# Performance work log

Hardware: AMD Instinct MI355X
Metric: run time of the kernel (lower is better)

Reference implementation:

```python
import jax, jax.numpy as jnp
import numpy as np

B, T, D_MODEL = 2, 1024, 1024
H, DEPTH = 8, 5
DH = D_MODEL // H


def setup_inputs() -> dict:
    key = jax.random.key(0)
    k_x, k_wp, k_bp, k_wv, k_wo = jax.random.split(key, 5)
    x = jax.random.normal(k_x, (B, T, D_MODEL), dtype=jnp.float32)
    # Parameters stored as [in, out] (y = x @ W + b), equivalent math to nn.Linear.
    Wp = jax.random.normal(k_wp, (D_MODEL, H * DEPTH), dtype=jnp.float32) * 0.02
    bp = jnp.zeros((H * DEPTH,), dtype=jnp.float32)
    Wv = jax.random.normal(k_wv, (D_MODEL, D_MODEL), dtype=jnp.float32) * 0.02
    Wo = jax.random.normal(k_wo, (D_MODEL, D_MODEL), dtype=jnp.float32) * 0.02
    return {"x": x, "Wp": Wp, "bp": bp, "Wv": Wv, "Wo": Wo}


def reference(x, Wp, bp, Wv, Wo):
    Bx, Tx, d = x.shape
    # soft binary path decisions: B,H,T,DEPTH
    paths = jax.nn.sigmoid(x @ Wp + bp)              # B,T,H*DEPTH
    paths = paths.reshape(Bx, Tx, H, DEPTH).transpose(0, 2, 1, 3)  # B,H,T,DEPTH
    # pairwise per-level agreement: B,H,Tq,Tk,DEPTH
    pq = paths[:, :, :, None, :]
    pk = paths[:, :, None, :, :]
    agree = pq * pk + (1.0 - pq) * (1.0 - pk)
    # shared-prefix length via cumprod over depth, summed
    sim = jnp.cumprod(agree, axis=-1).sum(axis=-1) / DEPTH  # B,H,Tq,Tk
    # causal mask
    mask = jnp.triu(jnp.ones((Tx, Tx), dtype=bool), k=1)
    sim = jnp.where(mask[None, None], -jnp.inf, sim)
    attn = jax.nn.softmax(sim, axis=-1)              # B,H,T,T
    V = (x @ Wv).reshape(Bx, Tx, H, DH).transpose(0, 2, 1, 3)  # B,H,T,dh
    ctx = jnp.einsum('bhqk,bhkd->bhqd', attn, V)
    ctx = ctx.transpose(0, 2, 1, 3).reshape(Bx, Tx, d)
    return ctx @ Wo
```

## Files before the change

kernel.cpp:

```cpp
#include <hip/hip_runtime.h>
#include <hip/hip_bf16.h>

#define B_ 2
#define T_ 1024
#define D_ 1024
#define H_ 8
#define DEPTH_ 5
#define DH_ 128

typedef short s16x8 __attribute__((ext_vector_type(8)));
typedef short s16x4 __attribute__((ext_vector_type(4)));
typedef float f32x4 __attribute__((ext_vector_type(4)));

__device__ inline short f2bf(float f) {
  __hip_bfloat16 h = __float2bfloat16(f);
  return *reinterpret_cast<short*>(&h);
}

typedef __attribute__((address_space(3))) unsigned int lds_u32_t;
typedef __attribute__((address_space(1))) unsigned int glb_u32_t;
__device__ __forceinline__ void glds16(const void* g, void* l) {
  __builtin_amdgcn_global_load_lds((const glb_u32_t*)g, (lds_u32_t*)l, 16, 0,
                                   0);
}

__global__ __launch_bounds__(256) void prep_kernel(
    const float* __restrict__ Wv, const float* __restrict__ Wo,
    const float* __restrict__ Wp, const float* __restrict__ x,
    short* __restrict__ WBt, short* __restrict__ Wot,
    short* __restrict__ xb) {
  int tid = threadIdx.x;
  if (blockIdx.z < 2) {
    const float* W = blockIdx.z ? Wo : Wv;
    short* Wt = blockIdx.z ? Wot : WBt;
    __shared__ float tile[64][65];
    int k0 = blockIdx.y * 64, n0 = blockIdx.x * 64;
#pragma unroll
    for (int i = 0; i < 4; ++i) {
      int idx = tid + i * 256;
      int r = idx >> 4, c4 = (idx & 15) * 4;
      float4 v = *(const float4*)&W[(size_t)(k0 + r) * D_ + n0 + c4];
      tile[r][c4 + 0] = v.x;
      tile[r][c4 + 1] = v.y;
      tile[r][c4 + 2] = v.z;
      tile[r][c4 + 3] = v.w;
    }
    __syncthreads();
#pragma unroll
    for (int j = 0; j < 2; ++j) {
      int idx = tid + j * 256;
      int n = idx >> 3, k8 = (idx & 7) * 8;
      s16x8 outv;
#pragma unroll
      for (int jj = 0; jj < 8; ++jj) outv[jj] = f2bf(tile[k8 + jj][n]);
      *(s16x8*)&Wt[(size_t)(n0 + n) * D_ + k0 + k8] = outv;
    }
  } else {
    int bid = blockIdx.y * 16 + blockIdx.x;
#pragma unroll
    for (int c = 0; c < 4; ++c) {
      size_t idx = (size_t)bid * 8192 + c * 2048 + tid * 8;
      float4 f0 = *(const float4*)&x[idx];
      float4 f1 = *(const float4*)&x[idx + 4];
      s16x8 v;
      v[0] = f2bf(f0.x); v[1] = f2bf(f0.y);
      v[2] = f2bf(f0.z); v[3] = f2bf(f0.w);
      v[4] = f2bf(f1.x); v[5] = f2bf(f1.y);
      v[6] = f2bf(f1.z); v[7] = f2bf(f1.w);
      *(s16x8*)&xb[idx] = v;
    }
    if (bid < 4) {
#pragma unroll
      for (int it = 0; it < 8; ++it) {
        int item = bid * 2048 + it * 256 + tid;
        int row = item >> 7, k8 = (item & 127) * 8;
        s16x8 v;
        if (row < H_ * DEPTH_) {
#pragma unroll
          for (int j = 0; j < 8; ++j)
            v[j] = f2bf(Wp[(size_t)(k8 + j) * (H_ * DEPTH_) + row]);
        } else {
#pragma unroll
          for (int j = 0; j < 8; ++j) v[j] = 0;
        }
        *(s16x8*)&WBt[(size_t)(1024 + row) * D_ + k8] = v;
      }
    }
  }
}

template <int MODE>
__global__ __launch_bounds__(256) void gemm128(
    const short* __restrict__ A, const short* __restrict__ Bt,
    float* __restrict__ Cf, const float* __restrict__ bp,
    short* __restrict__ Vt, float* __restrict__ paths_t) {
  __shared__ short As[64 * 128];
  __shared__ short Bs[64 * 128];
  const int K = D_;
  int tid = threadIdx.x;
  int bm = blockIdx.y << 6, bn = blockIdx.x << 6;
  int w = tid >> 6, lane = tid & 63;
  int wm = (w >> 1) * 32, wn = (w & 1) * 32;
  int g = lane >> 4, fr = lane & 15;
  f32x4 acc[2][2] = {{{0.f, 0.f, 0.f, 0.f}, {0.f, 0.f, 0.f, 0.f}},
                     {{0.f, 0.f, 0.f, 0.f}, {0.f, 0.f, 0.f, 0.f}}};

  int r4 = lane >> 4;
  int cg = lane & 15;
  const short* Asrc[4];
  const short* Bsrc[4];
  short* Adst[4];
  short* Bdst[4];
#pragma unroll
  for (int i = 0; i < 4; ++i) {
    int row = w * 16 + i * 4 + r4;
    int scol = (cg ^ (row & 15)) * 8;
    Asrc[i] = A + (size_t)(bm + row) * K + scol;
    Bsrc[i] = Bt + (size_t)(bn + row) * K + scol;
    Adst[i] = &As[(w * 16 + i * 4) * 128];
    Bdst[i] = &Bs[(w * 16 + i * 4) * 128];
  }

  for (int k0 = 0; k0 < K; k0 += 128) {
    __syncthreads();
#pragma unroll
    for (int i = 0; i < 4; ++i) {
      glds16(Asrc[i] + k0, Adst[i]);
      glds16(Bsrc[i] + k0, Bdst[i]);
    }
    __syncthreads();
#pragma unroll
    for (int ks = 0; ks < 4; ++ks) {
      int p = (((ks * 4 + g) ^ fr)) * 8;
      s16x8 a0 = *(const s16x8*)&As[(wm + fr) * 128 + p];
      s16x8 a1 = *(const s16x8*)&As[(wm + 16 + fr) * 128 + p];
      s16x8 b0 = *(const s16x8*)&Bs[(wn + fr) * 128 + p];
      s16x8 b1 = *(const s16x8*)&Bs[(wn + 16 + fr) * 128 + p];
      acc[0][0] = __builtin_amdgcn_mfma_f32_16x16x32_bf16(a0, b0, acc[0][0], 0, 0, 0);
      acc[0][1] = __builtin_amdgcn_mfma_f32_16x16x32_bf16(a0, b1, acc[0][1], 0, 0, 0);
      acc[1][0] = __builtin_amdgcn_mfma_f32_16x16x32_bf16(a1, b0, acc[1][0], 0, 0, 0);
      acc[1][1] = __builtin_amdgcn_mfma_f32_16x16x32_bf16(a1, b1, acc[1][1], 0, 0, 0);
    }
  }
  int col = lane & 15, rbase = (lane >> 4) * 4;
  if (MODE == 0) {
#pragma unroll
    for (int mi = 0; mi < 2; ++mi)
#pragma unroll
      for (int ni = 0; ni < 2; ++ni)
#pragma unroll
        for (int r = 0; r < 4; ++r)
          Cf[(size_t)(bm + wm + mi * 16 + rbase + r) * D_ + bn + wn +
             ni * 16 + col] = acc[mi][ni][r];
  } else if (bn < 1024) {
#pragma unroll
    for (int mi = 0; mi < 2; ++mi)
#pragma unroll
      for (int ni = 0; ni < 2; ++ni) {
        int m = bm + wm + mi * 16 + rbase;
        int n = bn + wn + ni * 16 + col;
        int b = m >> 10, t = m & (T_ - 1);
        int h = n >> 7, dh = n & (DH_ - 1);
        s16x4 v4;
#pragma unroll
        for (int r = 0; r < 4; ++r) v4[r] = f2bf(acc[mi][ni][r]);
        *(s16x4*)&Vt[((size_t)((b * H_ + h) * DH_ + dh)) * T_ + t] = v4;
      }
  } else {
#pragma unroll
    for (int ni = 0; ni < 2; ++ni) {
      int pn = wn + ni * 16 + col;
      if (pn < H_ * DEPTH_) {
        float bias = bp[pn];
        int h = pn / DEPTH_, d = pn % DEPTH_;
#pragma unroll
        for (int mi = 0; mi < 2; ++mi)
#pragma unroll
          for (int r = 0; r < 4; ++r) {
            int m = bm + wm + mi * 16 + rbase + r;
            int b = m >> 10, t = m & (T_ - 1);
            float p = 1.f / (1.f + __expf(-(acc[mi][ni][r] + bias)));
            paths_t[(((size_t)(b * H_ + h) * T_ + t) * DEPTH_) + d] = p;
          }
      }
    }
  }
}

#define LS2 136

__global__ __launch_bounds__(512) void attn_kernel(
    const float* __restrict__ paths_t, const short* __restrict__ Vt,
    short* __restrict__ ctxb) {
  int bh = blockIdx.y;
  int b = bh >> 3, h = bh & 7;
  int bx = blockIdx.x;
  int w = threadIdx.x >> 6, lane = threadIdx.x & 63;
  int g = lane >> 4, fr = lane & 15;

  __shared__ short Vs[DH_ * LS2];
  __shared__ short Ss[32 * LS2];
  __shared__ float lsum_s[32];

  const float* pb = paths_t + (size_t)bh * T_ * DEPTH_;
  const short* vb = Vt + (size_t)bh * DH_ * T_;

  for (int half = 0; half < 2; ++half) {
    int qt = half ? (31 - bx) : bx;
    int q0 = qt * 32;
    int nkt = (qt >> 2) + 1;

    float pq[4][DEPTH_], mq[4][DEPTH_];
#pragma unroll
    for (int j = 0; j < 4; ++j) {
      const float* qr = pb + (size_t)(q0 + w * 4 + j) * DEPTH_;
#pragma unroll
      for (int d = 0; d < DEPTH_; ++d) {
        pq[j][d] = qr[d];
        mq[j][d] = 1.f - pq[j][d];
      }
    }
    f32x4 acc[2] = {{0.f, 0.f, 0.f, 0.f}, {0.f, 0.f, 0.f, 0.f}};
    float part[4] = {};

    for (int kt = 0; kt < nkt; ++kt) {
      int k0 = kt * 128;
      __syncthreads();
#pragma unroll
      for (int i = 0; i < 4; ++i) {
        int c = threadIdx.x + i * 512;
        int dh = c >> 4, ko = (c & 15) * 8;
        *(s16x8*)&Vs[dh * LS2 + ko] =
            *(const s16x8*)&vb[(size_t)dh * T_ + k0 + ko];
      }
      int kA = k0 + lane, kB = k0 + 64 + lane;
      const float* krA = pb + (size_t)kA * DEPTH_;
      const float* krB = pb + (size_t)kB * DEPTH_;
      float pkA[DEPTH_], mkA[DEPTH_], pkB[DEPTH_], mkB[DEPTH_];
#pragma unroll
      for (int d = 0; d < DEPTH_; ++d) {
        pkA[d] = krA[d]; mkA[d] = 1.f - pkA[d];
        pkB[d] = krB[d]; mkB[d] = 1.f - pkB[d];
      }
#pragma unroll
      for (int j = 0; j < 4; ++j) {
        int qg = q0 + w * 4 + j;
        {
          float a0 = fmaf(pq[j][0], pkA[0], mq[j][0] * mkA[0]);
          float a1 = fmaf(pq[j][1], pkA[1], mq[j][1] * mkA[1]);
          float a2 = fmaf(pq[j][2], pkA[2], mq[j][2] * mkA[2]);
          float a3 = fmaf(pq[j][3], pkA[3], mq[j][3] * mkA[3]);
          float a4 = fmaf(pq[j][4], pkA[4], mq[j][4] * mkA[4]);
          float t4 = 1.f + a4;
          float t3 = fmaf(a3, t4, 1.f);
          float t2 = fmaf(a2, t3, 1.f);
          float t1 = fmaf(a1, t2, 1.f);
          float s = a0 * t1;
          float wv = (kA <= qg) ? __expf(s * 0.2f) : 0.f;
          part[j] += wv;
          Ss[(w * 4 + j) * LS2 + lane] = f2bf(wv);
        }
        {
          float a0 = fmaf(pq[j][0], pkB[0], mq[j][0] * mkB[0]);
          float a1 = fmaf(pq[j][1], pkB[1], mq[j][1] * mkB[1]);
          float a2 = fmaf(pq[j][2], pkB[2], mq[j][2] * mkB[2]);
          float a3 = fmaf(pq[j][3], pkB[3], mq[j][3] * mkB[3]);
          float a4 = fmaf(pq[j][4], pkB[4], mq[j][4] * mkB[4]);
          float t4 = 1.f + a4;
          float t3 = fmaf(a3, t4, 1.f);
          float t2 = fmaf(a2, t3, 1.f);
          float t1 = fmaf(a1, t2, 1.f);
          float s = a0 * t1;
          float wv = (kB <= qg) ? __expf(s * 0.2f) : 0.f;
          part[j] += wv;
          Ss[(w * 4 + j) * LS2 + 64 + lane] = f2bf(wv);
        }
      }
      __syncthreads();
#pragma unroll
      for (int ks = 0; ks < 4; ++ks) {
        int ko = ks * 32 + g * 8;
        s16x8 sa0 = *(const s16x8*)&Ss[fr * LS2 + ko];
        s16x8 sa1 = *(const s16x8*)&Ss[(16 + fr) * LS2 + ko];
        s16x8 vv = *(const s16x8*)&Vs[(w * 16 + fr) * LS2 + ko];
        acc[0] = __builtin_amdgcn_mfma_f32_16x16x32_bf16(sa0, vv, acc[0], 0, 0, 0);
        acc[1] = __builtin_amdgcn_mfma_f32_16x16x32_bf16(sa1, vv, acc[1], 0, 0, 0);
      }
    }
#pragma unroll
    for (int j = 0; j < 4; ++j) {
      float s = part[j];
#pragma unroll
      for (int off = 32; off >= 1; off >>= 1) s += __shfl_xor(s, off, 64);
      if (lane == j) lsum_s[w * 4 + j] = s;
    }
    __syncthreads();
    int col = lane & 15, rbase = g * 4;
#pragma unroll
    for (int qt2 = 0; qt2 < 2; ++qt2)
#pragma unroll
      for (int r = 0; r < 4; ++r) {
        int ql = qt2 * 16 + rbase + r;
        int dh = w * 16 + col;
        float val = acc[qt2][r] / lsum_s[ql];
        ctxb[(size_t)(b * T_ + q0 + ql) * D_ + h * DH_ + dh] = f2bf(val);
      }
  }
}

extern "C" void kernel_launch(void* const* d_in, const int* in_sizes, int n_in,
                              void* d_out, int out_size, void* d_ws,
                              size_t ws_size, hipStream_t stream) {
  const float* x = (const float*)d_in[0];
  const float* Wp = (const float*)d_in[1];
  const float* bp = (const float*)d_in[2];
  const float* Wv = (const float*)d_in[3];
  const float* Wo = (const float*)d_in[4];
  float* out = (float*)d_out;

  char* ws = (char*)d_ws;
  float* paths_t = (float*)ws;
  short* Vt = (short*)(ws + 327680);
  short* WBt = (short*)(ws + 4521984);
  short* Wot = (short*)(ws + 6750208);
  short* ctxb = (short*)(ws + 8847360);
  short* xb = (short*)(ws + 13041664);

  prep_kernel<<<dim3(16, 16, 3), 256, 0, stream>>>(Wv, Wo, Wp, x, WBt, Wot,
                                                   xb);
  gemm128<1><<<dim3(17, 32), 256, 0, stream>>>(xb, WBt, nullptr, bp, Vt,
                                               paths_t);
  attn_kernel<<<dim3(16, B_ * H_), 512, 0, stream>>>(paths_t, Vt, ctxb);
  gemm128<0><<<dim3(16, 32), 256, 0, stream>>>(ctxb, Wot, out, nullptr,
                                               nullptr, nullptr);
}
```

Before: 128.0 us.

## Fuse V-projection, attention and output GEMM into one cooperative persistent kernel

Replaces the three kernels that ran after prep (V/paths GEMM, attention, output GEMM) with a single cooperative kernel of 256 blocks that uses grid.sync between the V projection, attention and output-projection phases. The paths projection and sigmoid move into a fourth z-slice of the prep kernel, which converts x and Wp to bf16 on the fly. The GEMM phases switch from direct global-to-LDS loads with a swizzle to register-staged loads into padded LDS with 128x64 tiles. This is meant to remove launch overhead and idle gaps between kernels, at the cost of grid-wide barriers, a fixed grid of 256 blocks, and a simpler, non-async load path.

```diff
diff --git a/kernel.cpp b/kernel.cpp
--- a/kernel.cpp
+++ b/kernel.cpp
@@ -1,5 +1,8 @@
 #include <hip/hip_runtime.h>
 #include <hip/hip_bf16.h>
+#include <hip/hip_cooperative_groups.h>
+
+namespace cg = cooperative_groups;
 
 #define B_ 2
 #define T_ 1024
@@ -17,22 +20,18 @@
   return *reinterpret_cast<short*>(&h);
 }
 
-typedef __attribute__((address_space(3))) unsigned int lds_u32_t;
-typedef __attribute__((address_space(1))) unsigned int glb_u32_t;
-__device__ __forceinline__ void glds16(const void* g, void* l) {
-  __builtin_amdgcn_global_load_lds((const glb_u32_t*)g, (lds_u32_t*)l, 16, 0,
-                                   0);
-}
+#define MFMA16(a, b, c) __builtin_amdgcn_mfma_f32_16x16x32_bf16(a, b, c, 0, 0, 0)
 
 __global__ __launch_bounds__(256) void prep_kernel(
     const float* __restrict__ Wv, const float* __restrict__ Wo,
-    const float* __restrict__ Wp, const float* __restrict__ x,
-    short* __restrict__ WBt, short* __restrict__ Wot,
-    short* __restrict__ xb) {
+    const float* __restrict__ Wp, const float* __restrict__ bp,
+    const float* __restrict__ x, short* __restrict__ Wvt,
+    short* __restrict__ Wot, short* __restrict__ xb,
+    float* __restrict__ paths_t) {
   int tid = threadIdx.x;
   if (blockIdx.z < 2) {
     const float* W = blockIdx.z ? Wo : Wv;
-    short* Wt = blockIdx.z ? Wot : WBt;
+    short* Wt = blockIdx.z ? Wot : Wvt;
     __shared__ float tile[64][65];
     int k0 = blockIdx.y * 64, n0 = blockIdx.x * 64;
 #pragma unroll
@@ -55,7 +54,7 @@
       for (int jj = 0; jj < 8; ++jj) outv[jj] = f2bf(tile[k8 + jj][n]);
       *(s16x8*)&Wt[(size_t)(n0 + n) * D_ + k0 + k8] = outv;
     }
-  } else {
+  } else if (blockIdx.z == 2) {
     int bid = blockIdx.y * 16 + blockIdx.x;
 #pragma unroll
     for (int c = 0; c < 4; ++c) {
@@ -69,90 +68,132 @@
       v[6] = f2bf(f1.z); v[7] = f2bf(f1.w);
       *(s16x8*)&xb[idx] = v;
     }
-    if (bid < 4) {
-#pragma unroll
-      for (int it = 0; it < 8; ++it) {
-        int item = bid * 2048 + it * 256 + tid;
-        int row = item >> 7, k8 = (item & 127) * 8;
-        s16x8 v;
-        if (row < H_ * DEPTH_) {
-#pragma unroll
-          for (int j = 0; j < 8; ++j)
-            v[j] = f2bf(Wp[(size_t)(k8 + j) * (H_ * DEPTH_) + row]);
-        } else {
-#pragma unroll
-          for (int j = 0; j < 8; ++j) v[j] = 0;
-        }
-        *(s16x8*)&WBt[(size_t)(1024 + row) * D_ + k8] = v;
+  } else {
+    int bid = blockIdx.y * 16 + blockIdx.x;
+    if (bid >= 32) return;
+    __shared__ short As[64 * 72];
+    __shared__ short Bs[64 * 72];
+    int w = tid >> 6, lane = tid & 63;
+    int g = lane >> 4, fr = lane & 15;
+    int wm = (w >> 1) * 32, wn = (w & 1) * 32;
+    int bm = bid * 64;
+    f32x4 acc[2][2] = {{{0.f, 0.f, 0.f, 0.f}, {0.f, 0.f, 0.f, 0.f}},
+                       {{0.f, 0.f, 0.f, 0.f}, {0.f, 0.f, 0.f, 0.f}}};
+    for (int k0 = 0; k0 < D_; k0 += 64) {
+      s16x8 av[2];
+#pragma unroll
+      for (int i = 0; i < 2; ++i) {
+        int c = tid + i * 256;
+        int row = c >> 3, ko = (c & 7) * 8;
+        const float* p = &x[(size_t)(bm + row) * D_ + k0 + ko];
+        float4 f0 = *(const float4*)p, f1 = *(const float4*)(p + 4);
+        av[i][0] = f2bf(f0.x); av[i][1] = f2bf(f0.y);
+        av[i][2] = f2bf(f0.z); av[i][3] = f2bf(f0.w);
+        av[i][4] = f2bf(f1.x); av[i][5] = f2bf(f1.y);
+        av[i][6] = f2bf(f1.z); av[i][7] = f2bf(f1.w);
+      }
+      short bv[16];
+#pragma unroll
+      for (int j = 0; j < 16; ++j) {
+        int e = tid + j * 256;
+        int n = e & 63, r = e >> 6;
+        bv[j] = (n < H_ * DEPTH_) ? f2bf(Wp[(size_t)(k0 + r) * (H_ * DEPTH_) + n])
+                                  : (short)0;
+      }
+      __syncthreads();
+#pragma unroll
+      for (int i = 0; i < 2; ++i) {
+        int c = tid + i * 256;
+        int row = c >> 3, ko = (c & 7) * 8;
+        *(s16x8*)&As[row * 72 + ko] = av[i];
+      }
+#pragma unroll
+      for (int j = 0; j < 16; ++j) {
+        int e = tid + j * 256;
+        int n = e & 63, r = e >> 6;
+        Bs[n * 72 + r] = bv[j];
+      }
+      __syncthreads();
+#pragma unroll
+      for (int ks = 0; ks < 2; ++ks) {
+        int ko = ks * 32 + g * 8;
+        s16x8 a0 = *(const s16x8*)&As[(wm + fr) * 72 + ko];
+        s16x8 a1 = *(const s16x8*)&As[(wm + 16 + fr) * 72 + ko];
+        s16x8 b0 = *(const s16x8*)&Bs[(wn + fr) * 72 + ko];
+        s16x8 b1 = *(const s16x8*)&Bs[(wn + 16 + fr) * 72 + ko];
+        acc[0][0] = MFMA16(a0, b0, acc[0][0]);
+        acc[0][1] = MFMA16(a0, b1, acc[0][1]);
+        acc[1][0] = MFMA16(a1, b0, acc[1][0]);
+        acc[1][1] = MFMA16(a1, b1, acc[1][1]);
+      }
+    }
+    int col = fr, rbase = g * 4;
+#pragma unroll
+    for (int ni = 0; ni < 2; ++ni) {
+      int pn = wn + ni * 16 + col;
+      if (pn < H_ * DEPTH_) {
+        float bias = bp[pn];
+        int h = pn / DEPTH_, d = pn % DEPTH_;
+#pragma unroll
+        for (int mi = 0; mi < 2; ++mi)
+#pragma unroll
+          for (int r = 0; r < 4; ++r) {
+            int m = bm + wm + mi * 16 + rbase + r;
+            int b = m >> 10, t = m & (T_ - 1);
+            float pv = 1.f / (1.f + __expf(-(acc[mi][ni][r] + bias)));
+            paths_t[(((size_t)(b * H_ + h) * T_ + t) * DEPTH_) + d] = pv;
+          }
       }
     }
   }
 }
 
-template <int MODE>
-__global__ __launch_bounds__(256) void gemm128(
-    const short* __restrict__ A, const short* __restrict__ Bt,
-    float* __restrict__ Cf, const float* __restrict__ bp,
-    short* __restrict__ Vt, float* __restrict__ paths_t) {
-  __shared__ short As[64 * 128];
-  __shared__ short Bs[64 * 128];
-  const int K = D_;
+#define LS2 136
+#define SMEM_BYTES 43648
+
+__global__ __launch_bounds__(512) void fused_kernel(
+    const short* __restrict__ xb, const short* __restrict__ Wvt,
+    short* __restrict__ Vt, const float* __restrict__ paths_t,
+    const short* __restrict__ Wot, short* __restrict__ ctxb,
+    float* __restrict__ outp) {
+  cg::grid_group grid = cg::this_grid();
+  __shared__ __align__(16) char smem[SMEM_BYTES];
   int tid = threadIdx.x;
-  int bm = blockIdx.y << 6, bn = blockIdx.x << 6;
   int w = tid >> 6, lane = tid & 63;
-  int wm = (w >> 1) * 32, wn = (w & 1) * 32;
   int g = lane >> 4, fr = lane & 15;
-  f32x4 acc[2][2] = {{{0.f, 0.f, 0.f, 0.f}, {0.f, 0.f, 0.f, 0.f}},
-                     {{0.f, 0.f, 0.f, 0.f}, {0.f, 0.f, 0.f, 0.f}}};
-
-  int r4 = lane >> 4;
-  int cg = lane & 15;
-  const short* Asrc[4];
-  const short* Bsrc[4];
-  short* Adst[4];
-  short* Bdst[4];
-#pragma unroll
-  for (int i = 0; i < 4; ++i) {
-    int row = w * 16 + i * 4 + r4;
-    int scol = (cg ^ (row & 15)) * 8;
-    Asrc[i] = A + (size_t)(bm + row) * K + scol;
-    Bsrc[i] = Bt + (size_t)(bn + row) * K + scol;
-    Adst[i] = &As[(w * 16 + i * 4) * 128];
-    Bdst[i] = &Bs[(w * 16 + i * 4) * 128];
-  }
-
-  for (int k0 = 0; k0 < K; k0 += 128) {
-    __syncthreads();
-#pragma unroll
-    for (int i = 0; i < 4; ++i) {
-      glds16(Asrc[i] + k0, Adst[i]);
-      glds16(Bsrc[i] + k0, Bdst[i]);
-    }
-    __syncthreads();
-#pragma unroll
-    for (int ks = 0; ks < 4; ++ks) {
-      int p = (((ks * 4 + g) ^ fr)) * 8;
-      s16x8 a0 = *(const s16x8*)&As[(wm + fr) * 128 + p];
-      s16x8 a1 = *(const s16x8*)&As[(wm + 16 + fr) * 128 + p];
-      s16x8 b0 = *(const s16x8*)&Bs[(wn + fr) * 128 + p];
-      s16x8 b1 = *(const s16x8*)&Bs[(wn + 16 + fr) * 128 + p];
-      acc[0][0] = __builtin_amdgcn_mfma_f32_16x16x32_bf16(a0, b0, acc[0][0], 0, 0, 0);
-      acc[0][1] = __builtin_amdgcn_mfma_f32_16x16x32_bf16(a0, b1, acc[0][1], 0, 0, 0);
-      acc[1][0] = __builtin_amdgcn_mfma_f32_16x16x32_bf16(a1, b0, acc[1][0], 0, 0, 0);
-      acc[1][1] = __builtin_amdgcn_mfma_f32_16x16x32_bf16(a1, b1, acc[1][1], 0, 0, 0);
-    }
-  }
-  int col = lane & 15, rbase = (lane >> 4) * 4;
-  if (MODE == 0) {
-#pragma unroll
-    for (int mi = 0; mi < 2; ++mi)
-#pragma unroll
-      for (int ni = 0; ni < 2; ++ni)
-#pragma unroll
-        for (int r = 0; r < 4; ++r)
-          Cf[(size_t)(bm + wm + mi * 16 + rbase + r) * D_ + bn + wn +
-             ni * 16 + col] = acc[mi][ni][r];
-  } else if (bn < 1024) {
+  int u = blockIdx.x;
+
+  {
+    short* As = (short*)smem;
+    short* Bs = As + 128 * 72;
+    int bm = (u & 15) << 7, bn = (u >> 4) << 6;
+    int wm = (w >> 1) * 32, wn = (w & 1) * 32;
+    int srow = tid >> 3, sko = (tid & 7) * 8;
+    f32x4 acc[2][2] = {{{0.f, 0.f, 0.f, 0.f}, {0.f, 0.f, 0.f, 0.f}},
+                       {{0.f, 0.f, 0.f, 0.f}, {0.f, 0.f, 0.f, 0.f}}};
+    for (int k0 = 0; k0 < D_; k0 += 64) {
+      s16x8 av0 = *(const s16x8*)&xb[(size_t)(bm + srow) * D_ + k0 + sko];
+      s16x8 av1 = *(const s16x8*)&xb[(size_t)(bm + 64 + srow) * D_ + k0 + sko];
+      s16x8 bv = *(const s16x8*)&Wvt[(size_t)(bn + srow) * D_ + k0 + sko];
+      __syncthreads();
+      *(s16x8*)&As[srow * 72 + sko] = av0;
+      *(s16x8*)&As[(64 + srow) * 72 + sko] = av1;
+      *(s16x8*)&Bs[srow * 72 + sko] = bv;
+      __syncthreads();
+#pragma unroll
+      for (int ks = 0; ks < 2; ++ks) {
+        int ko = ks * 32 + g * 8;
+        s16x8 a0 = *(const s16x8*)&As[(wm + fr) * 72 + ko];
+        s16x8 a1 = *(const s16x8*)&As[(wm + 16 + fr) * 72 + ko];
+        s16x8 b0 = *(const s16x8*)&Bs[(wn + fr) * 72 + ko];
+        s16x8 b1 = *(const s16x8*)&Bs[(wn + 16 + fr) * 72 + ko];
+        acc[0][0] = MFMA16(a0, b0, acc[0][0]);
+        acc[0][1] = MFMA16(a0, b1, acc[0][1]);
+        acc[1][0] = MFMA16(a1, b0, acc[1][0]);
+        acc[1][1] = MFMA16(a1, b1, acc[1][1]);
+      }
+    }
+    int col = fr, rbase = g * 4;
 #pragma unroll
     for (int mi = 0; mi < 2; ++mi)
 #pragma unroll
@@ -166,145 +207,165 @@
         for (int r = 0; r < 4; ++r) v4[r] = f2bf(acc[mi][ni][r]);
         *(s16x4*)&Vt[((size_t)((b * H_ + h) * DH_ + dh)) * T_ + t] = v4;
       }
-  } else {
-#pragma unroll
-    for (int ni = 0; ni < 2; ++ni) {
-      int pn = wn + ni * 16 + col;
-      if (pn < H_ * DEPTH_) {
-        float bias = bp[pn];
-        int h = pn / DEPTH_, d = pn % DEPTH_;
-#pragma unroll
-        for (int mi = 0; mi < 2; ++mi)
-#pragma unroll
-          for (int r = 0; r < 4; ++r) {
-            int m = bm + wm + mi * 16 + rbase + r;
-            int b = m >> 10, t = m & (T_ - 1);
-            float p = 1.f / (1.f + __expf(-(acc[mi][ni][r] + bias)));
-            paths_t[(((size_t)(b * H_ + h) * T_ + t) * DEPTH_) + d] = p;
+  }
+  __threadfence();
+  grid.sync();
+
+  {
+    short* Vs = (short*)smem;
+    short* Ss = Vs + DH_ * LS2;
+    float* lsum_s = (float*)(Ss + 32 * LS2);
+    int bh = u >> 4, bx = u & 15;
+    int b = bh >> 3, h = bh & 7;
+    const float* pb = paths_t + (size_t)bh * T_ * DEPTH_;
+    const short* vb = Vt + (size_t)bh * DH_ * T_;
+
+    for (int half = 0; half < 2; ++half) {
+      int qt = half ? (31 - bx) : bx;
+      int q0 = qt * 32;
+      int nkt = (qt >> 2) + 1;
+
+      float pq[4][DEPTH_], mq[4][DEPTH_];
+#pragma unroll
+      for (int j = 0; j < 4; ++j) {
+        const float* qr = pb + (size_t)(q0 + w * 4 + j) * DEPTH_;
+#pragma unroll
+        for (int d = 0; d < DEPTH_; ++d) {
+          pq[j][d] = qr[d];
+          mq[j][d] = 1.f - pq[j][d];
+        }
+      }
+      f32x4 acc[2] = {{0.f, 0.f, 0.f, 0.f}, {0.f, 0.f, 0.f, 0.f}};
+      float part[4] = {};
+
+      for (int kt = 0; kt < nkt; ++kt) {
+        int k0 = kt * 128;
+        __syncthreads();
+#pragma unroll
+        for (int i = 0; i < 4; ++i) {
+          int c = tid + i * 512;
+          int dh = c >> 4, ko = (c & 15) * 8;
+          *(s16x8*)&Vs[dh * LS2 + ko] =
+              *(const s16x8*)&vb[(size_t)dh * T_ + k0 + ko];
+        }
+        int kA = k0 + lane, kB = k0 + 64 + lane;
+        const float* krA = pb + (size_t)kA * DEPTH_;
+        const float* krB = pb + (size_t)kB * DEPTH_;
+        float pkA[DEPTH_], mkA[DEPTH_], pkB[DEPTH_], mkB[DEPTH_];
+#pragma unroll
+        for (int d = 0; d < DEPTH_; ++d) {
+          pkA[d] = krA[d]; mkA[d] = 1.f - pkA[d];
+          pkB[d] = krB[d]; mkB[d] = 1.f - pkB[d];
+        }
+#pragma unroll
+        for (int j = 0; j < 4; ++j) {
+          int qg = q0 + w * 4 + j;
+          {
+            float a0 = fmaf(pq[j][0], pkA[0], mq[j][0] * mkA[0]);
+            float a1 = fmaf(pq[j][1], pkA[1], mq[j][1] * mkA[1]);
+            float a2 = fmaf(pq[j][2], pkA[2], mq[j][2] * mkA[2]);
+            float a3 = fmaf(pq[j][3], pkA[3], mq[j][3] * mkA[3]);
+            float a4 = fmaf(pq[j][4], pkA[4], mq[j][4] * mkA[4]);
+            float t4 = 1.f + a4;
+            float t3 = fmaf(a3, t4, 1.f);
+            float t2 = fmaf(a2, t3, 1.f);
+            float t1 = fmaf(a1, t2, 1.f);
+            float s = a0 * t1;
+            float wv = (kA <= qg) ? __expf(s * 0.2f) : 0.f;
+            part[j] += wv;
+            Ss[(w * 4 + j) * LS2 + lane] = f2bf(wv);
           }
-      }
+          {
+            float a0 = fmaf(pq[j][0], pkB[0], mq[j][0] * mkB[0]);
+            float a1 = fmaf(pq[j][1], pkB[1], mq[j][1] * mkB[1]);
+            float a2 = fmaf(pq[j][2], pkB[2], mq[j][2] * mkB[2]);
+            float a3 = fmaf(pq[j][3], pkB[3], mq[j][3] * mkB[3]);
+            float a4 = fmaf(pq[j][4], pkB[4], mq[j][4] * mkB[4]);
+            float t4 = 1.f + a4;
+            float t3 = fmaf(a3, t4, 1.f);
+            float t2 = fmaf(a2, t3, 1.f);
+            float t1 = fmaf(a1, t2, 1.f);
+            float s = a0 * t1;
+            float wv = (kB <= qg) ? __expf(s * 0.2f) : 0.f;
+            part[j] += wv;
+            Ss[(w * 4 + j) * LS2 + 64 + lane] = f2bf(wv);
+          }
+        }
+        __syncthreads();
+#pragma unroll
+        for (int ks = 0; ks < 4; ++ks) {
+          int ko = ks * 32 + g * 8;
+          s16x8 sa0 = *(const s16x8*)&Ss[fr * LS2 + ko];
+          s16x8 sa1 = *(const s16x8*)&Ss[(16 + fr) * LS2 + ko];
+          s16x8 vv = *(const s16x8*)&Vs[(w * 16 + fr) * LS2 + ko];
+          acc[0] = MFMA16(sa0, vv, acc[0]);
+          acc[1] = MFMA16(sa1, vv, acc[1]);
+        }
+      }
+#pragma unroll
+      for (int j = 0; j < 4; ++j) {
+        float s = part[j];
+#pragma unroll
+        for (int off = 32; off >= 1; off >>= 1) s += __shfl_xor(s, off, 64);
+        if (lane == j) lsum_s[w * 4 + j] = s;
+      }
+      __syncthreads();
+      int col = fr, rbase = g * 4;
+#pragma unroll
+      for (int qt2 = 0; qt2 < 2; ++qt2)
+#pragma unroll
+        for (int r = 0; r < 4; ++r) {
+          int ql = qt2 * 16 + rbase + r;
+          int dh = w * 16 + col;
+          float val = acc[qt2][r] / lsum_s[ql];
+          ctxb[(size_t)(b * T_ + q0 + ql) * D_ + h * DH_ + dh] = f2bf(val);
+        }
+      __syncthreads();
     }
   }
-}
-
-#define LS2 136
-
-__global__ __launch_bounds__(512) void attn_kernel(
-    const float* __restrict__ paths_t, const short* __restrict__ Vt,
-    short* __restrict__ ctxb) {
-  int bh = blockIdx.y;
-  int b = bh >> 3, h = bh & 7;
-  int bx = blockIdx.x;
-  int w = threadIdx.x >> 6, lane = threadIdx.x & 63;
-  int g = lane >> 4, fr = lane & 15;
-
-  __shared__ short Vs[DH_ * LS2];
-  __shared__ short Ss[32 * LS2];
-  __shared__ float lsum_s[32];
-
-  const float* pb = paths_t + (size_t)bh * T_ * DEPTH_;
-  const short* vb = Vt + (size_t)bh * DH_ * T_;
-
-  for (int half = 0; half < 2; ++half) {
-    int qt = half ? (31 - bx) : bx;
-    int q0 = qt * 32;
-    int nkt = (qt >> 2) + 1;
-
-    float pq[4][DEPTH_], mq[4][DEPTH_];
-#pragma unroll
-    for (int j = 0; j < 4; ++j) {
-      const float* qr = pb + (size_t)(q0 + w * 4 + j) * DEPTH_;
-#pragma unroll
-      for (int d = 0; d < DEPTH_; ++d) {
-        pq[j][d] = qr[d];
-        mq[j][d] = 1.f - pq[j][d];
-      }
-    }
-    f32x4 acc[2] = {{0.f, 0.f, 0.f, 0.f}, {0.f, 0.f, 0.f, 0.f}};
-    float part[4] = {};
-
-    for (int kt = 0; kt < nkt; ++kt) {
-      int k0 = kt * 128;
-      __syncthreads();
-#pragma unroll
-      for (int i = 0; i < 4; ++i) {
-        int c = threadIdx.x + i * 512;
-        int dh = c >> 4, ko = (c & 15) * 8;
-        *(s16x8*)&Vs[dh * LS2 + ko] =
-            *(const s16x8*)&vb[(size_t)dh * T_ + k0 + ko];
-      }
-      int kA = k0 + lane, kB = k0 + 64 + lane;
-      const float* krA = pb + (size_t)kA * DEPTH_;
-      const float* krB = pb + (size_t)kB * DEPTH_;
-      float pkA[DEPTH_], mkA[DEPTH_], pkB[DEPTH_], mkB[DEPTH_];
-#pragma unroll
-      for (int d = 0; d < DEPTH_; ++d) {
-        pkA[d] = krA[d]; mkA[d] = 1.f - pkA[d];
-        pkB[d] = krB[d]; mkB[d] = 1.f - pkB[d];
-      }
-#pragma unroll
-      for (int j = 0; j < 4; ++j) {
-        int qg = q0 + w * 4 + j;
-        {
-          float a0 = fmaf(pq[j][0], pkA[0], mq[j][0] * mkA[0]);
-          float a1 = fmaf(pq[j][1], pkA[1], mq[j][1] * mkA[1]);
-          float a2 = fmaf(pq[j][2], pkA[2], mq[j][2] * mkA[2]);
-          float a3 = fmaf(pq[j][3], pkA[3], mq[j][3] * mkA[3]);
-          float a4 = fmaf(pq[j][4], pkA[4], mq[j][4] * mkA[4]);
-          float t4 = 1.f + a4;
-          float t3 = fmaf(a3, t4, 1.f);
-          float t2 = fmaf(a2, t3, 1.f);
-          float t1 = fmaf(a1, t2, 1.f);
-          float s = a0 * t1;
-          float wv = (kA <= qg) ? __expf(s * 0.2f) : 0.f;
-          part[j] += wv;
-          Ss[(w * 4 + j) * LS2 + lane] = f2bf(wv);
-        }
-        {
-          float a0 = fmaf(pq[j][0], pkB[0], mq[j][0] * mkB[0]);
-          float a1 = fmaf(pq[j][1], pkB[1], mq[j][1] * mkB[1]);
-          float a2 = fmaf(pq[j][2], pkB[2], mq[j][2] * mkB[2]);
-          float a3 = fmaf(pq[j][3], pkB[3], mq[j][3] * mkB[3]);
-          float a4 = fmaf(pq[j][4], pkB[4], mq[j][4] * mkB[4]);
-          float t4 = 1.f + a4;
-          float t3 = fmaf(a3, t4, 1.f);
-          float t2 = fmaf(a2, t3, 1.f);
-          float t1 = fmaf(a1, t2, 1.f);
-          float s = a0 * t1;
-          float wv = (kB <= qg) ? __expf(s * 0.2f) : 0.f;
-          part[j] += wv;
-          Ss[(w * 4 + j) * LS2 + 64 + lane] = f2bf(wv);
-        }
-      }
-      __syncthreads();
-#pragma unroll
-      for (int ks = 0; ks < 4; ++ks) {
+  __threadfence();
+  grid.sync();
+
+  {
+    short* As = (short*)smem;
+    short* Bs = As + 128 * 72;
+    int bm = (u & 15) << 7, bn = (u >> 4) << 6;
+    int wm = (w >> 1) * 32, wn = (w & 1) * 32;
+    int srow = tid >> 3, sko = (tid & 7) * 8;
+    f32x4 acc[2][2] = {{{0.f, 0.f, 0.f, 0.f}, {0.f, 0.f, 0.f, 0.f}},
+                       {{0.f, 0.f, 0.f, 0.f}, {0.f, 0.f, 0.f, 0.f}}};
+    for (int k0 = 0; k0 < D_; k0 += 64) {
+      s16x8 av0 = *(const s16x8*)&ctxb[(size_t)(bm + srow) * D_ + k0 + sko];
+      s16x8 av1 =
+          *(const s16x8*)&ctxb[(size_t)(bm + 64 + srow) * D_ + k0 + sko];
+      s16x8 bv = *(const s16x8*)&Wot[(size_t)(bn + srow) * D_ + k0 + sko];
+      __syncthreads();
+      *(s16x8*)&As[srow * 72 + sko] = av0;
+      *(s16x8*)&As[(64 + srow) * 72 + sko] = av1;
+      *(s16x8*)&Bs[srow * 72 + sko] = bv;
+      __syncthreads();
+#pragma unroll
+      for (int ks = 0; ks < 2; ++ks) {
         int ko = ks * 32 + g * 8;
-        s16x8 sa0 = *(const s16x8*)&Ss[fr * LS2 + ko];
-        s16x8 sa1 = *(const s16x8*)&Ss[(16 + fr) * LS2 + ko];
-        s16x8 vv = *(const s16x8*)&Vs[(w * 16 + fr) * LS2 + ko];
-        acc[0] = __builtin_amdgcn_mfma_f32_16x16x32_bf16(sa0, vv, acc[0], 0, 0, 0);
-        acc[1] = __builtin_amdgcn_mfma_f32_16x16x32_bf16(sa1, vv, acc[1], 0, 0, 0);
-      }
-    }
-#pragma unroll
-    for (int j = 0; j < 4; ++j) {
-      float s = part[j];
-#pragma unroll
-      for (int off = 32; off >= 1; off >>= 1) s += __shfl_xor(s, off, 64);
-      if (lane == j) lsum_s[w * 4 + j] = s;
-    }
-    __syncthreads();
-    int col = lane & 15, rbase = g * 4;
-#pragma unroll
-    for (int qt2 = 0; qt2 < 2; ++qt2)
-#pragma unroll
-      for (int r = 0; r < 4; ++r) {
-        int ql = qt2 * 16 + rbase + r;
-        int dh = w * 16 + col;
-        float val = acc[qt2][r] / lsum_s[ql];
-        ctxb[(size_t)(b * T_ + q0 + ql) * D_ + h * DH_ + dh] = f2bf(val);
-      }
+        s16x8 a0 = *(const s16x8*)&As[(wm + fr) * 72 + ko];
+        s16x8 a1 = *(const s16x8*)&As[(wm + 16 + fr) * 72 + ko];
+        s16x8 b0 = *(const s16x8*)&Bs[(wn + fr) * 72 + ko];
+        s16x8 b1 = *(const s16x8*)&Bs[(wn + 16 + fr) * 72 + ko];
+        acc[0][0] = MFMA16(a0, b0, acc[0][0]);
+        acc[0][1] = MFMA16(a0, b1, acc[0][1]);
+        acc[1][0] = MFMA16(a1, b0, acc[1][0]);
+        acc[1][1] = MFMA16(a1, b1, acc[1][1]);
+      }
+    }
+    int col = fr, rbase = g * 4;
+#pragma unroll
+    for (int mi = 0; mi < 2; ++mi)
+#pragma unroll
+      for (int ni = 0; ni < 2; ++ni)
+#pragma unroll
+        for (int r = 0; r < 4; ++r)
+          outp[(size_t)(bm + wm + mi * 16 + rbase + r) * D_ + bn + wn +
+               ni * 16 + col] = acc[mi][ni][r];
   }
 }
 
@@ -321,16 +382,15 @@
   char* ws = (char*)d_ws;
   float* paths_t = (float*)ws;
   short* Vt = (short*)(ws + 327680);
-  short* WBt = (short*)(ws + 4521984);
-  short* Wot = (short*)(ws + 6750208);
-  short* ctxb = (short*)(ws + 8847360);
-  short* xb = (short*)(ws + 13041664);
-
-  prep_kernel<<<dim3(16, 16, 3), 256, 0, stream>>>(Wv, Wo, Wp, x, WBt, Wot,
-                                                   xb);
-  gemm128<1><<<dim3(17, 32), 256, 0, stream>>>(xb, WBt, nullptr, bp, Vt,
-                                               paths_t);
-  attn_kernel<<<dim3(16, B_ * H_), 512, 0, stream>>>(paths_t, Vt, ctxb);
-  gemm128<0><<<dim3(16, 32), 256, 0, stream>>>(ctxb, Wot, out, nullptr,
-                                               nullptr, nullptr);
+  short* Wvt = (short*)(ws + 4521984);
+  short* Wot = (short*)(ws + 6619136);
+  short* ctxb = (short*)(ws + 8716288);
+  short* xb = (short*)(ws + 12910592);
+
+  prep_kernel<<<dim3(16, 16, 4), 256, 0, stream>>>(Wv, Wo, Wp, bp, x, Wvt,
+                                                   Wot, xb, paths_t);
+  void* kargs[] = {(void*)&xb,  (void*)&Wvt,  (void*)&Vt, (void*)&paths_t,
+                   (void*)&Wot, (void*)&ctxb, (void*)&out};
+  hipLaunchCooperativeKernel((void*)fused_kernel, dim3(256), dim3(512), kargs,
+                             0, stream);
 }
```

Result: slower. 341.6 us (+167.0%).

## Move path projection into prep kernel and async-load V tiles in attention

Applied to the files above, without the earlier changes.

The sigmoid path projection (x @ Wp) moves out of the V-projection GEMM into a new 32-block branch of the prep kernel. That branch converts x and Wp to bf16 on the fly and writes paths_t directly, so the V GEMM loses its 17th column of mostly-padded work and the Wp transpose/pad step. In the attention kernel, V tiles are now loaded with global_load_lds into an XOR-swizzled 128-wide LDS layout, issued between the path loads, instead of synchronous register copies. The added path branch runs a serial 16-step K loop in only 32 blocks with scalar strided Wp reads, which may lengthen the prep kernel's critical path.

```diff
diff --git a/kernel.cpp b/kernel.cpp
--- a/kernel.cpp
+++ b/kernel.cpp
@@ -17,6 +17,8 @@
   return *reinterpret_cast<short*>(&h);
 }
 
+#define MFMA16(a, b, c) __builtin_amdgcn_mfma_f32_16x16x32_bf16(a, b, c, 0, 0, 0)
+
 typedef __attribute__((address_space(3))) unsigned int lds_u32_t;
 typedef __attribute__((address_space(1))) unsigned int glb_u32_t;
 __device__ __forceinline__ void glds16(const void* g, void* l) {
@@ -26,13 +28,14 @@
 
 __global__ __launch_bounds__(256) void prep_kernel(
     const float* __restrict__ Wv, const float* __restrict__ Wo,
-    const float* __restrict__ Wp, const float* __restrict__ x,
-    short* __restrict__ WBt, short* __restrict__ Wot,
-    short* __restrict__ xb) {
+    const float* __restrict__ Wp, const float* __restrict__ bp,
+    const float* __restrict__ x, short* __restrict__ Wvt,
+    short* __restrict__ Wot, short* __restrict__ xb,
+    float* __restrict__ paths_t) {
   int tid = threadIdx.x;
   if (blockIdx.z < 2) {
     const float* W = blockIdx.z ? Wo : Wv;
-    short* Wt = blockIdx.z ? Wot : WBt;
+    short* Wt = blockIdx.z ? Wot : Wvt;
     __shared__ float tile[64][65];
     int k0 = blockIdx.y * 64, n0 = blockIdx.x * 64;
 #pragma unroll
@@ -55,7 +58,7 @@
       for (int jj = 0; jj < 8; ++jj) outv[jj] = f2bf(tile[k8 + jj][n]);
       *(s16x8*)&Wt[(size_t)(n0 + n) * D_ + k0 + k8] = outv;
     }
-  } else {
+  } else if (blockIdx.z == 2) {
     int bid = blockIdx.y * 16 + blockIdx.x;
 #pragma unroll
     for (int c = 0; c < 4; ++c) {
@@ -69,21 +72,82 @@
       v[6] = f2bf(f1.z); v[7] = f2bf(f1.w);
       *(s16x8*)&xb[idx] = v;
     }
-    if (bid < 4) {
-#pragma unroll
-      for (int it = 0; it < 8; ++it) {
-        int item = bid * 2048 + it * 256 + tid;
-        int row = item >> 7, k8 = (item & 127) * 8;
-        s16x8 v;
-        if (row < H_ * DEPTH_) {
-#pragma unroll
-          for (int j = 0; j < 8; ++j)
-            v[j] = f2bf(Wp[(size_t)(k8 + j) * (H_ * DEPTH_) + row]);
-        } else {
-#pragma unroll
-          for (int j = 0; j < 8; ++j) v[j] = 0;
-        }
-        *(s16x8*)&WBt[(size_t)(1024 + row) * D_ + k8] = v;
+  } else {
+    int bid = blockIdx.y * 16 + blockIdx.x;
+    if (bid >= 32) return;
+    __shared__ short As[64 * 72];
+    __shared__ short Bs[64 * 72];
+    int w = tid >> 6, lane = tid & 63;
+    int g = lane >> 4, fr = lane & 15;
+    int wm = (w >> 1) * 32, wn = (w & 1) * 32;
+    int bm = bid * 64;
+    f32x4 acc[2][2] = {{{0.f, 0.f, 0.f, 0.f}, {0.f, 0.f, 0.f, 0.f}},
+                       {{0.f, 0.f, 0.f, 0.f}, {0.f, 0.f, 0.f, 0.f}}};
+    for (int k0 = 0; k0 < D_; k0 += 64) {
+      s16x8 av[2];
+#pragma unroll
+      for (int i = 0; i < 2; ++i) {
+        int c = tid + i * 256;
+        int row = c >> 3, ko = (c & 7) * 8;
+        const float* p = &x[(size_t)(bm + row) * D_ + k0 + ko];
+        float4 f0 = *(const float4*)p, f1 = *(const float4*)(p + 4);
+        av[i][0] = f2bf(f0.x); av[i][1] = f2bf(f0.y);
+        av[i][2] = f2bf(f0.z); av[i][3] = f2bf(f0.w);
+        av[i][4] = f2bf(f1.x); av[i][5] = f2bf(f1.y);
+        av[i][6] = f2bf(f1.z); av[i][7] = f2bf(f1.w);
+      }
+      short bv[16];
+#pragma unroll
+      for (int j = 0; j < 16; ++j) {
+        int e = tid + j * 256;
+        int n = e & 63, r = e >> 6;
+        bv[j] = (n < H_ * DEPTH_)
+                    ? f2bf(Wp[(size_t)(k0 + r) * (H_ * DEPTH_) + n])
+                    : (short)0;
+      }
+      __syncthreads();
+#pragma unroll
+      for (int i = 0; i < 2; ++i) {
+        int c = tid + i * 256;
+        int row = c >> 3, ko = (c & 7) * 8;
+        *(s16x8*)&As[row * 72 + ko] = av[i];
+      }
+#pragma unroll
+      for (int j = 0; j < 16; ++j) {
+        int e = tid + j * 256;
+        int n = e & 63, r = e >> 6;
+        Bs[n * 72 + r] = bv[j];
+      }
+      __syncthreads();
+#pragma unroll
+      for (int ks = 0; ks < 2; ++ks) {
+        int ko = ks * 32 + g * 8;
+        s16x8 a0 = *(const s16x8*)&As[(wm + fr) * 72 + ko];
+        s16x8 a1 = *(const s16x8*)&As[(wm + 16 + fr) * 72 + ko];
+        s16x8 b0 = *(const s16x8*)&Bs[(wn + fr) * 72 + ko];
+        s16x8 b1 = *(const s16x8*)&Bs[(wn + 16 + fr) * 72 + ko];
+        acc[0][0] = MFMA16(a0, b0, acc[0][0]);
+        acc[0][1] = MFMA16(a0, b1, acc[0][1]);
+        acc[1][0] = MFMA16(a1, b0, acc[1][0]);
+        acc[1][1] = MFMA16(a1, b1, acc[1][1]);
+      }
+    }
+    int col = fr, rbase = g * 4;
+#pragma unroll
+    for (int ni = 0; ni < 2; ++ni) {
+      int pn = wn + ni * 16 + col;
+      if (pn < H_ * DEPTH_) {
+        float bias = bp[pn];
+        int h = pn / DEPTH_, d = pn % DEPTH_;
+#pragma unroll
+        for (int mi = 0; mi < 2; ++mi)
+#pragma unroll
+          for (int r = 0; r < 4; ++r) {
+            int m = bm + wm + mi * 16 + rbase + r;
+            int b = m >> 10, t = m & (T_ - 1);
+            float pv = 1.f / (1.f + __expf(-(acc[mi][ni][r] + bias)));
+            paths_t[(((size_t)(b * H_ + h) * T_ + t) * DEPTH_) + d] = pv;
+          }
       }
     }
   }
@@ -92,8 +156,7 @@
 template <int MODE>
 __global__ __launch_bounds__(256) void gemm128(
     const short* __restrict__ A, const short* __restrict__ Bt,
-    float* __restrict__ Cf, const float* __restrict__ bp,
-    short* __restrict__ Vt, float* __restrict__ paths_t) {
+    float* __restrict__ Cf, short* __restrict__ Vt) {
   __shared__ short As[64 * 128];
   __shared__ short Bs[64 * 128];
   const int K = D_;
@@ -131,15 +194,15 @@
     __syncthreads();
 #pragma unroll
     for (int ks = 0; ks < 4; ++ks) {
-      int p = (((ks * 4 + g) ^ fr)) * 8;
+      int p = ((ks * 4 + g) ^ fr) * 8;
       s16x8 a0 = *(const s16x8*)&As[(wm + fr) * 128 + p];
       s16x8 a1 = *(const s16x8*)&As[(wm + 16 + fr) * 128 + p];
       s16x8 b0 = *(const s16x8*)&Bs[(wn + fr) * 128 + p];
       s16x8 b1 = *(const s16x8*)&Bs[(wn + 16 + fr) * 128 + p];
-      acc[0][0] = __builtin_amdgcn_mfma_f32_16x16x32_bf16(a0, b0, acc[0][0], 0, 0, 0);
-      acc[0][1] = __builtin_amdgcn_mfma_f32_16x16x32_bf16(a0, b1, acc[0][1], 0, 0, 0);
-      acc[1][0] = __builtin_amdgcn_mfma_f32_16x16x32_bf16(a1, b0, acc[1][0], 0, 0, 0);
-      acc[1][1] = __builtin_amdgcn_mfma_f32_16x16x32_bf16(a1, b1, acc[1][1], 0, 0, 0);
+      acc[0][0] = MFMA16(a0, b0, acc[0][0]);
+      acc[0][1] = MFMA16(a0, b1, acc[0][1]);
+      acc[1][0] = MFMA16(a1, b0, acc[1][0]);
+      acc[1][1] = MFMA16(a1, b1, acc[1][1]);
     }
   }
   int col = lane & 15, rbase = (lane >> 4) * 4;
@@ -152,7 +215,7 @@
         for (int r = 0; r < 4; ++r)
           Cf[(size_t)(bm + wm + mi * 16 + rbase + r) * D_ + bn + wn +
              ni * 16 + col] = acc[mi][ni][r];
-  } else if (bn < 1024) {
+  } else {
 #pragma unroll
     for (int mi = 0; mi < 2; ++mi)
 #pragma unroll
@@ -166,24 +229,6 @@
         for (int r = 0; r < 4; ++r) v4[r] = f2bf(acc[mi][ni][r]);
         *(s16x4*)&Vt[((size_t)((b * H_ + h) * DH_ + dh)) * T_ + t] = v4;
       }
-  } else {
-#pragma unroll
-    for (int ni = 0; ni < 2; ++ni) {
-      int pn = wn + ni * 16 + col;
-      if (pn < H_ * DEPTH_) {
-        float bias = bp[pn];
-        int h = pn / DEPTH_, d = pn % DEPTH_;
-#pragma unroll
-        for (int mi = 0; mi < 2; ++mi)
-#pragma unroll
-          for (int r = 0; r < 4; ++r) {
-            int m = bm + wm + mi * 16 + rbase + r;
-            int b = m >> 10, t = m & (T_ - 1);
-            float p = 1.f / (1.f + __expf(-(acc[mi][ni][r] + bias)));
-            paths_t[(((size_t)(b * H_ + h) * T_ + t) * DEPTH_) + d] = p;
-          }
-      }
-    }
   }
 }
 
@@ -198,12 +243,23 @@
   int w = threadIdx.x >> 6, lane = threadIdx.x & 63;
   int g = lane >> 4, fr = lane & 15;
 
-  __shared__ short Vs[DH_ * LS2];
+  __shared__ short Vs[DH_ * 128];
   __shared__ short Ss[32 * LS2];
   __shared__ float lsum_s[32];
 
   const float* pb = paths_t + (size_t)bh * T_ * DEPTH_;
   const short* vb = Vt + (size_t)bh * DH_ * T_;
+
+  int r4 = lane >> 4, cg = lane & 15;
+  const short* Vsrc[4];
+  short* Vdst[4];
+#pragma unroll
+  for (int i = 0; i < 4; ++i) {
+    int row = w * 16 + i * 4 + r4;
+    int scol = (cg ^ (row & 15)) * 8;
+    Vsrc[i] = vb + (size_t)row * T_ + scol;
+    Vdst[i] = &Vs[(w * 16 + i * 4) * 128];
+  }
 
   for (int half = 0; half < 2; ++half) {
     int qt = half ? (31 - bx) : bx;
@@ -226,21 +282,21 @@
     for (int kt = 0; kt < nkt; ++kt) {
       int k0 = kt * 128;
       __syncthreads();
-#pragma unroll
-      for (int i = 0; i < 4; ++i) {
-        int c = threadIdx.x + i * 512;
-        int dh = c >> 4, ko = (c & 15) * 8;
-        *(s16x8*)&Vs[dh * LS2 + ko] =
-            *(const s16x8*)&vb[(size_t)dh * T_ + k0 + ko];
-      }
       int kA = k0 + lane, kB = k0 + 64 + lane;
       const float* krA = pb + (size_t)kA * DEPTH_;
       const float* krB = pb + (size_t)kB * DEPTH_;
       float pkA[DEPTH_], mkA[DEPTH_], pkB[DEPTH_], mkB[DEPTH_];
 #pragma unroll
       for (int d = 0; d < DEPTH_; ++d) {
-        pkA[d] = krA[d]; mkA[d] = 1.f - pkA[d];
-        pkB[d] = krB[d]; mkB[d] = 1.f - pkB[d];
+        pkA[d] = krA[d];
+        pkB[d] = krB[d];
+      }
+#pragma unroll
+      for (int i = 0; i < 4; ++i) glds16(Vsrc[i] + k0, Vdst[i]);
+#pragma unroll
+      for (int d = 0; d < DEPTH_; ++d) {
+        mkA[d] = 1.f - pkA[d];
+        mkB[d] = 1.f - pkB[d];
       }
 #pragma unroll
       for (int j = 0; j < 4; ++j) {
@@ -280,11 +336,12 @@
 #pragma unroll
       for (int ks = 0; ks < 4; ++ks) {
         int ko = ks * 32 + g * 8;
+        int sl = ((ks * 4 + g) ^ fr) * 8;
         s16x8 sa0 = *(const s16x8*)&Ss[fr * LS2 + ko];
         s16x8 sa1 = *(const s16x8*)&Ss[(16 + fr) * LS2 + ko];
-        s16x8 vv = *(const s16x8*)&Vs[(w * 16 + fr) * LS2 + ko];
-        acc[0] = __builtin_amdgcn_mfma_f32_16x16x32_bf16(sa0, vv, acc[0], 0, 0, 0);
-        acc[1] = __builtin_amdgcn_mfma_f32_16x16x32_bf16(sa1, vv, acc[1], 0, 0, 0);
+        s16x8 vv = *(const s16x8*)&Vs[(w * 16 + fr) * 128 + sl];
+        acc[0] = MFMA16(sa0, vv, acc[0]);
+        acc[1] = MFMA16(sa1, vv, acc[1]);
       }
     }
 #pragma unroll
@@ -295,7 +352,7 @@
       if (lane == j) lsum_s[w * 4 + j] = s;
     }
     __syncthreads();
-    int col = lane & 15, rbase = g * 4;
+    int col = fr, rbase = g * 4;
 #pragma unroll
     for (int qt2 = 0; qt2 < 2; ++qt2)
 #pragma unroll
@@ -305,6 +362,7 @@
         float val = acc[qt2][r] / lsum_s[ql];
         ctxb[(size_t)(b * T_ + q0 + ql) * D_ + h * DH_ + dh] = f2bf(val);
       }
+    __syncthreads();
   }
 }
 
@@ -321,16 +379,14 @@
   char* ws = (char*)d_ws;
   float* paths_t = (float*)ws;
   short* Vt = (short*)(ws + 327680);
-  short* WBt = (short*)(ws + 4521984);
-  short* Wot = (short*)(ws + 6750208);
-  short* ctxb = (short*)(ws + 8847360);
-  short* xb = (short*)(ws + 13041664);
-
-  prep_kernel<<<dim3(16, 16, 3), 256, 0, stream>>>(Wv, Wo, Wp, x, WBt, Wot,
-                                                   xb);
-  gemm128<1><<<dim3(17, 32), 256, 0, stream>>>(xb, WBt, nullptr, bp, Vt,
-                                               paths_t);
+  short* Wvt = (short*)(ws + 4521984);
+  short* Wot = (short*)(ws + 6619136);
+  short* ctxb = (short*)(ws + 8716288);
+  short* xb = (short*)(ws + 12910592);
+
+  prep_kernel<<<dim3(16, 16, 4), 256, 0, stream>>>(Wv, Wo, Wp, bp, x, Wvt,
+                                                   Wot, xb, paths_t);
+  gemm128<1><<<dim3(16, 32), 256, 0, stream>>>(xb, Wvt, nullptr, Vt);
   attn_kernel<<<dim3(16, B_ * H_), 512, 0, stream>>>(paths_t, Vt, ctxb);
-  gemm128<0><<<dim3(16, 32), 256, 0, stream>>>(ctxb, Wot, out, nullptr,
-                                               nullptr, nullptr);
-}
+  gemm128<0><<<dim3(16, 32), 256, 0, stream>>>(ctxb, Wot, out, nullptr);
+}
```

Measured after the change: 183.3 us. 1.43x slower.
